# Optimization experiments

Measured on AMD Instinct MI355X. Metric: run time of the kernel, lower is better.

## Reference

```python
import jax, jax.numpy as jnp
import numpy as np
from jax import lax

EPS = 1e-5

# Straight-through binarization (sign forward, identity grad) as in BNN repos
@jax.custom_vjp
def binarize(x):
    return jnp.sign(x)

def _bin_fwd(x):
    return jnp.sign(x), None

def _bin_bwd(_, g):
    return (g,)

binarize.defvjp(_bin_fwd, _bin_bwd)

def hardtanh(x):
    return jnp.clip(x, -1.0, 1.0)

def bn2d(x, g, b):
    # training-mode batch norm over (N,H,W), biased variance (torch behavior)
    m = x.mean(axis=(0, 2, 3), keepdims=True)
    v = x.var(axis=(0, 2, 3), keepdims=True)
    return (x - m) * lax.rsqrt(v + EPS) * g[None, :, None, None] + b[None, :, None, None]

def bn1d(x, g, b):
    m = x.mean(axis=0, keepdims=True)
    v = x.var(axis=0, keepdims=True)
    return (x - m) * lax.rsqrt(v + EPS) * g[None, :] + b[None, :]

def conv(x, w, stride=1, padding='VALID', groups=1):
    return lax.conv_general_dilated(
        x, w, window_strides=(stride, stride), padding=padding,
        dimension_numbers=('NCHW', 'OIHW', 'NCHW'), feature_group_count=groups)

def setup_inputs() -> dict:
    key = jax.random.key(0)
    ks = jax.random.split(key, 16)
    B, C, H = 16, 128, 56
    E = C * 6          # 768 expanded channels
    SE = C // 8        # 16 SE bottleneck
    r = lambda k, sh: (jax.random.normal(k, sh, dtype=jnp.float32) * 0.1)
    return {
        'x': jax.random.normal(ks[0], (B, C, H, H), dtype=jnp.float32),
        'w1': r(ks[1], (E, C, 1, 1)), 'g1': jnp.ones((E,)), 'b1': jnp.zeros((E,)),
        'w2': r(ks[2], (E, 1, 3, 3)), 'g2': jnp.ones((E,)), 'b2': jnp.zeros((E,)),
        'w3': r(ks[3], (C, E, 1, 1)), 'g3': jnp.ones((C,)), 'b3': jnp.zeros((C,)),
        'g_res': jnp.ones((C,)), 'b_res': jnp.zeros((C,)),
        'g_se1': jnp.ones((C,)), 'b_se1': jnp.zeros((C,)),
        'w_fc2': r(ks[4], (SE, C)), 'bias_fc2': jnp.zeros((SE,)),
        'g_se2': jnp.ones((SE,)), 'b_se2': jnp.zeros((SE,)),
        'w_fc3': r(ks[5], (C, SE)), 'bias_fc3': jnp.zeros((C,)),
        'g_se3': jnp.ones((C,)), 'b_se3': jnp.zeros((C,)),
    }

def reference(x, w1, g1, b1, w2, g2, b2, w3, g3, b3, g_res, b_res,
              g_se1, b_se1, w_fc2, bias_fc2, g_se2, b_se2,
              w_fc3, bias_fc3, g_se3, b_se3):
    residual = x
    E = w1.shape[0]
    # 1x1 binarized pointwise expand
    out = conv(binarize(x), binarize(w1))
    out = hardtanh(bn2d(out, g1, b1))
    # 3x3 binarized depthwise (groups = E), stride 1, pad 1
    out = conv(binarize(out), binarize(w2), stride=1, padding='SAME', groups=E)
    out = hardtanh(bn2d(out, g2, b2))
    # 1x1 binarized pointwise project
    out = conv(binarize(out), binarize(w3))
    out = hardtanh(bn2d(out, g3, b3))
    # SE path: global avg pool -> BN -> hardtanh -> binarized FCs -> sigmoid gate
    se = out.mean(axis=(2, 3), keepdims=True)              # [B,C,1,1]
    se = hardtanh(bn2d(se, g_se1, b_se1))[:, :, 0, 0]      # [B,C]
    se = binarize(se) @ binarize(w_fc2).T + bias_fc2
    se = hardtanh(bn1d(se, g_se2, b_se2))
    se = binarize(se) @ binarize(w_fc3).T + bias_fc3
    se = jax.nn.sigmoid(bn1d(se, g_se3, b_se3))            # [B,C]
    out = out * se[:, :, None, None]                       # einsum 'bjik,bj->bjik'
    # residual (stride==1, ch_in==ch_out) + BN + hardtanh
    out = hardtanh(bn2d(out + residual, g_res, b_res))
    return out
```

## Files before the change

kernel.cpp:

```cpp
#include <hip/hip_runtime.h>
#include <stdint.h>

#define BATCH 16
#define CIN   128
#define HH    56
#define HW    3136
#define NPOS  50176
#define ECH   768
#define CH1   49

__device__ uint32_t g_X[NPOS * 8];
__device__ uint32_t g_Wp1[ECH * 8];
__device__ uint32_t g_sw2u[9 * 192];
__device__ uint32_t g_Wp3[CIN * 48];
__device__ int8_t   g_bin1[(size_t)NPOS * ECH];
__device__ int8_t   g_z2[(size_t)NPOS * ECH];
__device__ int16_t  g_z3[(size_t)NPOS * CIN];

__device__ int32_t  g_S1[ECH], g_SS1[ECH];
__device__ int32_t  g_S2[ECH], g_SS2[ECH];
__device__ int32_t  g_S3[CIN];
__device__ unsigned long long g_SS3[CIN];
__device__ double   g_Pm[BATCH * CIN];
__device__ double   g_Ys[CIN], g_Yss[CIN];
__device__ float    g_se[BATCH * CIN];

__device__ __forceinline__ int tdot128(const uint32_t* xn, const uint32_t* xsg,
                                       const uint32_t* wn, const uint32_t* wsg) {
  int pc = 0, mc = 0;
#pragma unroll
  for (int k = 0; k < 4; ++k) {
    uint32_t nab = xn[k] & wn[k];
    uint32_t sx  = xsg[k] ^ wsg[k];
    pc += __popc(nab);
    mc += __popc(nab & sx);
  }
  return pc - 2 * mc;
}

__global__ __launch_bounds__(256) void k_pack(const float* __restrict__ x,
                                              const float* __restrict__ w1,
                                              const float* __restrict__ w2,
                                              const float* __restrict__ w3) {
  __shared__ uint8_t sh[CIN * 64];
  __shared__ uint32_t pk[64 * 8];
  int b = blockIdx.x, t = threadIdx.x;
  if (b < 784) {
    int pos0 = b * 64;
    int n = pos0 / HW, hw0 = pos0 % HW;
    const float* xp = x + (size_t)n * CIN * HW + hw0;
    int lc = t >> 6, lp = t & 63;
#pragma unroll 8
    for (int c4 = 0; c4 < CIN; c4 += 4) {
      float v = xp[(size_t)(c4 + lc) * HW + lp];
      uint8_t code = (v != 0.f) ? (v < 0.f ? 3u : 1u) : 0u;
      sh[(c4 + lc) * 64 + lp] = code;
    }
    __syncthreads();
    int w = t >> 6, p = t & 63;
    uint32_t nw = 0, sw = 0;
#pragma unroll
    for (int i = 0; i < 32; ++i) {
      uint32_t code = sh[(w * 32 + i) * 64 + p];
      nw |= (code & 1u) << i;
      sw |= ((code >> 1) & 1u) << i;
    }
    pk[p * 8 + w] = nw;
    pk[p * 8 + 4 + w] = sw;
    __syncthreads();
    uint32_t* dst = g_X + (size_t)b * 512;
    dst[t] = pk[t];
    dst[t + 256] = pk[t + 256];
  } else if (b < 796) {
    int wid = (b - 784) * 4 + (t >> 6);
    int lane = t & 63;
    for (int e = wid; e < ECH; e += 48) {
      const float* wp = w1 + (size_t)e * CIN;
      float v0 = wp[lane];
      float v1 = wp[64 + lane];
      unsigned long long n0 = __ballot(v0 != 0.f);
      unsigned long long s0 = __ballot(v0 < 0.f);
      unsigned long long n1 = __ballot(v1 != 0.f);
      unsigned long long s1 = __ballot(v1 < 0.f);
      if (lane == 0) {
        uint32_t* d = g_Wp1 + e * 8;
        d[0] = (uint32_t)n0; d[1] = (uint32_t)(n0 >> 32);
        d[2] = (uint32_t)n1; d[3] = (uint32_t)(n1 >> 32);
        d[4] = (uint32_t)s0; d[5] = (uint32_t)(s0 >> 32);
        d[6] = (uint32_t)s1; d[7] = (uint32_t)(s1 >> 32);
      }
    }
  } else if (b < 804) {
    int wid = (b - 796) * 4 + (t >> 6);
    int lane = t & 63;
    for (int o = wid; o < CIN; o += 32) {
      const float* wp = w3 + (size_t)o * ECH;
      uint32_t* d = g_Wp3 + o * 48;
#pragma unroll
      for (int k = 0; k < 12; ++k) {
        float v = wp[k * 64 + lane];
        unsigned long long nm = __ballot(v != 0.f);
        unsigned long long sm = __ballot(v < 0.f);
        if (lane == 0) {
          d[2 * k]     = (uint32_t)nm; d[2 * k + 1]      = (uint32_t)(nm >> 32);
          d[24 + 2 * k] = (uint32_t)sm; d[24 + 2 * k + 1] = (uint32_t)(sm >> 32);
        }
      }
    }
  } else if (b == 804) {
    if (t < 192) {
      int d = t;
#pragma unroll
      for (int tap = 0; tap < 9; ++tap) {
        uint32_t wd = 0;
#pragma unroll
        for (int bb = 0; bb < 4; ++bb) {
          float v = w2[(size_t)(4 * d + bb) * 9 + tap];
          int s8 = (v > 0.f) - (v < 0.f);
          wd |= ((uint32_t)(uint8_t)(int8_t)s8) << (8 * bb);
        }
        g_sw2u[tap * 192 + d] = wd;
      }
    }
  } else {
    for (int i = t; i < ECH; i += 256) { g_S1[i] = 0; g_SS1[i] = 0; g_S2[i] = 0; g_SS2[i] = 0; }
    if (t < CIN) { g_S3[t] = 0; g_SS3[t] = 0ull; g_Ys[t] = 0.0; g_Yss[t] = 0.0; }
  }
}

__global__ __launch_bounds__(256) void k_conv1_stats() {
  __shared__ uint32_t xsh[CH1 * 8];
  int b = blockIdx.x, t = threadIdx.x;
  size_t pos0 = (size_t)b * CH1;
  for (int i = t; i < CH1 * 8; i += 256) xsh[i] = g_X[pos0 * 8 + i];
  uint32_t w[3][8];
#pragma unroll
  for (int j = 0; j < 3; ++j) {
    int e = t + j * 256;
#pragma unroll
    for (int k = 0; k < 8; ++k) w[j][k] = g_Wp1[e * 8 + k];
  }
  __syncthreads();
  int s[3] = {0,0,0}, ss[3] = {0,0,0};
  for (int p = 0; p < CH1; ++p) {
    uint32_t xv[8];
#pragma unroll
    for (int k = 0; k < 8; ++k) xv[k] = xsh[p * 8 + k];
#pragma unroll
    for (int j = 0; j < 3; ++j) {
      int z = tdot128(xv, xv + 4, w[j], w[j] + 4);
      s[j] += z; ss[j] += z * z;
    }
  }
#pragma unroll
  for (int j = 0; j < 3; ++j) {
    int e = t + j * 256;
    atomicAdd(&g_S1[e], s[j]); atomicAdd(&g_SS1[e], ss[j]);
  }
}

__global__ __launch_bounds__(256) void k_conv1_bin(const float* __restrict__ g1,
                                                   const float* __restrict__ b1) {
  __shared__ uint32_t xsh[CH1 * 8];
  int b = blockIdx.x, t = threadIdx.x;
  size_t pos0 = (size_t)b * CH1;
  for (int i = t; i < CH1 * 8; i += 256) xsh[i] = g_X[pos0 * 8 + i];
  uint32_t w[3][8]; float A[3], Bc[3];
#pragma unroll
  for (int j = 0; j < 3; ++j) {
    int e = t + j * 256;
#pragma unroll
    for (int k = 0; k < 8; ++k) w[j][k] = g_Wp1[e * 8 + k];
    double m = (double)g_S1[e] / (double)NPOS;
    double v = (double)g_SS1[e] / (double)NPOS - m * m;
    float inv = (float)(1.0 / sqrt(v + 1e-5));
    A[j] = inv * g1[e]; Bc[j] = b1[e] - (float)m * A[j];
  }
  __syncthreads();
  for (int p = 0; p < CH1; ++p) {
    uint32_t xv[8];
#pragma unroll
    for (int k = 0; k < 8; ++k) xv[k] = xsh[p * 8 + k];
    size_t rowoff = (pos0 + p) * ECH;
#pragma unroll
    for (int j = 0; j < 3; ++j) {
      int z = tdot128(xv, xv + 4, w[j], w[j] + 4);
      float u = fmaf((float)z, A[j], Bc[j]);
      g_bin1[rowoff + t + j * 256] = (int8_t)((u > 0.f) - (u < 0.f));
    }
  }
}

__global__ __launch_bounds__(384) void k_dw() {
  int b = blockIdx.x, t = threadIdx.x;
  int n = b / HH, h = b % HH;
  int half = t >= 192 ? 1 : 0;
  int d = t - half * 192;
  int wbeg = half * 28;

  int ws[9][4];
#pragma unroll
  for (int tap = 0; tap < 9; ++tap) {
    uint32_t wd = g_sw2u[tap * 192 + d];
#pragma unroll
    for (int bb = 0; bb < 4; ++bb) ws[tap][bb] = (int)(int8_t)(uint8_t)(wd >> (8 * bb));
  }

  const uint32_t* binu = (const uint32_t*)g_bin1;
  int rowM = (n * HW + h * HH) * 192 + d;
  bool okT = (h > 0), okB = (h < HH - 1);
  int rT = okT ? rowM - HH * 192 : rowM;
  int rB = okB ? rowM + HH * 192 : rowM;
  uint32_t mT = okT ? 0xffffffffu : 0u;
  uint32_t mB = okB ? 0xffffffffu : 0u;

  uint32_t At, Am, Ab, Bt, Bm, Bb, Ct, Cm, Cb, Dt, Dm, Db, Et, Em, Eb;

#define LOADC(c, vt, vm, vb) do {                                   \
    int cs_ = (c) < 0 ? 0 : ((c) > 55 ? 55 : (c));                  \
    int off_ = cs_ * 192;                                           \
    uint32_t mc_ = ((unsigned)(c) < 56u) ? 0xffffffffu : 0u;        \
    vt = binu[rT + off_];                                           \
    vm = binu[rowM + off_];                                         \
    vb = binu[rB + off_];                                           \
    vt &= (mc_ & mT); vm &= mc_; vb &= (mc_ & mB);                  \
  } while (0)

  LOADC(wbeg - 1, At, Am, Ab);
  LOADC(wbeg,     Bt, Bm, Bb);
  LOADC(wbeg + 1, Ct, Cm, Cb);
  LOADC(wbeg + 2, Dt, Dm, Db);
  LOADC(wbeg + 3, Et, Em, Eb);

  int s0 = 0, s1 = 0, s2 = 0, s3 = 0, q0 = 0, q1 = 0, q2 = 0, q3 = 0;
  uint32_t* z2u = (uint32_t*)g_z2;

#define ACC1(val, tap) do {                                            \
    z0 += __mul24((int)(int8_t)(uint8_t)((val)      ), ws[tap][0]);    \
    z1 += __mul24((int)(int8_t)(uint8_t)((val) >>  8), ws[tap][1]);    \
    z2v+= __mul24((int)(int8_t)(uint8_t)((val) >> 16), ws[tap][2]);    \
    z3 += __mul24((int)(int8_t)(uint8_t)((val) >> 24), ws[tap][3]);    \
  } while (0)

  for (int i = 0; i < 28; ++i) {
    int w = wbeg + i;
    int z0 = 0, z1 = 0, z2v = 0, z3 = 0;
    ACC1(At, 0); ACC1(Bt, 1); ACC1(Ct, 2);
    ACC1(Am, 3); ACC1(Bm, 4); ACC1(Cm, 5);
    ACC1(Ab, 6); ACC1(Bb, 7); ACC1(Cb, 8);
    uint32_t od = (uint32_t)(z0 & 0xff) | ((uint32_t)(z1 & 0xff) << 8) |
                  ((uint32_t)(z2v & 0xff) << 16) | ((uint32_t)(z3 & 0xff) << 24);
    z2u[rowM + w * 192] = od;
    s0 += z0; s1 += z1; s2 += z2v; s3 += z3;
    q0 += __mul24(z0, z0); q1 += __mul24(z1, z1);
    q2 += __mul24(z2v, z2v); q3 += __mul24(z3, z3);
    At = Bt; Am = Bm; Ab = Bb;
    Bt = Ct; Bm = Cm; Bb = Cb;
    Ct = Dt; Cm = Dm; Cb = Db;
    Dt = Et; Dm = Em; Db = Eb;
    LOADC(w + 4, Et, Em, Eb);
  }
#undef LOADC
#undef ACC1

  __shared__ int shS[ECH], shQ[ECH];
  for (int i = t; i < ECH; i += 384) { shS[i] = 0; shQ[i] = 0; }
  __syncthreads();
  atomicAdd(&shS[4 * d + 0], s0); atomicAdd(&shS[4 * d + 1], s1);
  atomicAdd(&shS[4 * d + 2], s2); atomicAdd(&shS[4 * d + 3], s3);
  atomicAdd(&shQ[4 * d + 0], q0); atomicAdd(&shQ[4 * d + 1], q1);
  atomicAdd(&shQ[4 * d + 2], q2); atomicAdd(&shQ[4 * d + 3], q3);
  __syncthreads();
  for (int i = t; i < ECH; i += 384) {
    atomicAdd(&g_S2[i], shS[i]);
    atomicAdd(&g_SS2[i], shQ[i]);
  }
}

__global__ __launch_bounds__(256) void k_conv3(const float* __restrict__ g2,
                                               const float* __restrict__ b2) {
  __shared__ uint32_t pk[64 * 49];
  __shared__ float A2s[ECH], B2s[ECH];
  int b = blockIdx.x, t = threadIdx.x;
  int pos0 = b * 64;
  for (int e = t; e < ECH; e += 256) {
    double m = (double)g_S2[e] / (double)NPOS;
    double v = (double)g_SS2[e] / (double)NPOS - m * m;
    float inv = (float)(1.0 / sqrt(v + 1e-5));
    float Af = inv * g2[e]; A2s[e] = Af; B2s[e] = b2[e] - (float)m * Af;
  }
  __syncthreads();
  int p = t & 63, q = t >> 6;
  const uint4* src = (const uint4*)(g_z2 + (size_t)(pos0 + p) * ECH + q * 192);
  uint32_t nw[6] = {0,0,0,0,0,0}, sw[6] = {0,0,0,0,0,0};
#pragma unroll
  for (int v = 0; v < 12; ++v) {
    uint4 d4 = src[v];
    uint32_t dws[4] = {d4.x, d4.y, d4.z, d4.w};
#pragma unroll
    for (int dw = 0; dw < 4; ++dw) {
      uint32_t dv = dws[dw];
#pragma unroll
      for (int by = 0; by < 4; ++by) {
        int j = v * 16 + dw * 4 + by;
        int c = q * 192 + j;
        float zz = (float)(int)(int8_t)(dv >> (by * 8));
        float u = fmaf(zz, A2s[c], B2s[c]);
        uint32_t bit = 1u << (j & 31);
        if (u != 0.0f) { nw[j >> 5] |= bit; if (u < 0.0f) sw[j >> 5] |= bit; }
      }
    }
  }
#pragma unroll
  for (int k = 0; k < 6; ++k) {
    pk[p * 49 + q * 6 + k] = nw[k];
    pk[p * 49 + 24 + q * 6 + k] = sw[k];
  }
  __syncthreads();
  uint32_t an[24], asx[24];
#pragma unroll
  for (int k = 0; k < 24; ++k) { an[k] = pk[p * 49 + k]; asx[k] = pk[p * 49 + 24 + k]; }
  int n_img = pos0 / HW;
  int hw = pos0 % HW + p;
  for (int i = 0; i < 32; ++i) {
    int o = __builtin_amdgcn_readfirstlane(q * 32 + i);
    const uint32_t* wr = &g_Wp3[o * 48];
    int pc = 0, mc = 0;
#pragma unroll
    for (int k = 0; k < 24; ++k) {
      uint32_t nab = an[k] & wr[k];
      uint32_t sx  = asx[k] ^ wr[24 + k];
      pc += __popc(nab); mc += __popc(nab & sx);
    }
    int z = pc - 2 * mc;
    g_z3[((size_t)n_img * CIN + o) * HW + hw] = (int16_t)z;
  }
}

__global__ __launch_bounds__(256) void k_stats3() {
  int b = blockIdx.x;
  int n = b >> 7, c = b & 127, t = threadIdx.x;
  const uint32_t* zp = (const uint32_t*)(g_z3 + ((size_t)n * CIN + c) * HW);
  int s = 0, ss = 0;
  for (int i = t; i < 1568; i += 256) {
    uint32_t dv = zp[i];
    int a  = (int)(int16_t)(dv & 0xffff);
    int b2 = (int)(int16_t)(dv >> 16);
    s += a + b2; ss += a * a + b2 * b2;
  }
  __shared__ int rs[256], rss[256];
  rs[t] = s; rss[t] = ss; __syncthreads();
  for (int st = 128; st > 0; st >>= 1) {
    if (t < st) { rs[t] += rs[t + st]; rss[t] += rss[t + st]; }
    __syncthreads();
  }
  if (t == 0) {
    atomicAdd(&g_S3[c], rs[0]);
    atomicAdd(&g_SS3[c], (unsigned long long)(unsigned)rss[0]);
  }
}

__global__ __launch_bounds__(256) void k_pool(const float* __restrict__ g3,
                                              const float* __restrict__ b3) {
  int b = blockIdx.x;
  int n = b >> 7, c = b & 127, t = threadIdx.x;
  __shared__ double red[256];
  __shared__ float par[2];
  if (t == 0) {
    double m = (double)g_S3[c] / (double)NPOS;
    double v = (double)g_SS3[c] / (double)NPOS - m * m;
    float inv = (float)(1.0 / sqrt(v + 1e-5));
    float Af = inv * g3[c]; par[0] = Af; par[1] = b3[c] - (float)m * Af;
  }
  __syncthreads();
  float Af = par[0], Bc = par[1];
  const int16_t* zp = g_z3 + ((size_t)n * CIN + c) * HW;
  double acc = 0.0;
  for (int i = t; i < HW; i += 256) {
    float u = fmaf((float)zp[i], Af, Bc);
    u = fminf(1.f, fmaxf(-1.f, u));
    acc += (double)u;
  }
  red[t] = acc; __syncthreads();
  for (int s2 = 128; s2 > 0; s2 >>= 1) { if (t < s2) red[t] += red[t + s2]; __syncthreads(); }
  if (t == 0) g_Pm[b] = red[0];
}

__global__ __launch_bounds__(256) void k_se(const float* __restrict__ g_se1, const float* __restrict__ b_se1,
                                            const float* __restrict__ w_fc2, const float* __restrict__ bias_fc2,
                                            const float* __restrict__ g_se2, const float* __restrict__ b_se2,
                                            const float* __restrict__ w_fc3, const float* __restrict__ bias_fc3,
                                            const float* __restrict__ g_se3, const float* __restrict__ b_se3) {
  __shared__ float s1b[16 * 128];
  __shared__ float s2b[16 * 16];
  __shared__ float zfc[16 * 16];
  int t = threadIdx.x;
  if (t < 128) {
    int c = t; double sum = 0, ssum = 0; double vals[16];
    for (int n = 0; n < 16; ++n) {
      double v = g_Pm[n * 128 + c] / 3136.0;
      vals[n] = v; sum += v; ssum += v * v;
    }
    double m = sum / 16.0, var = ssum / 16.0 - m * m;
    double inv = 1.0 / sqrt(var + 1e-5);
    for (int n = 0; n < 16; ++n) {
      float u = (float)((vals[n] - m) * inv * (double)g_se1[c] + (double)b_se1[c]);
      u = fminf(1.f, fmaxf(-1.f, u));
      s1b[n * 128 + c] = (float)((u > 0.f) - (u < 0.f));
    }
  }
  __syncthreads();
  {
    int n = t >> 4, k = t & 15;
    float acc = bias_fc2[k];
    for (int c = 0; c < 128; ++c) {
      float w = w_fc2[k * 128 + c];
      acc += s1b[n * 128 + c] * (float)((w > 0.f) - (w < 0.f));
    }
    zfc[n * 16 + k] = acc;
  }
  __syncthreads();
  if (t < 16) {
    int k = t; double sum = 0, ssum = 0;
    for (int n = 0; n < 16; ++n) { double v = zfc[n * 16 + k]; sum += v; ssum += v * v; }
    double m = sum / 16.0, var = ssum / 16.0 - m * m;
    double inv = 1.0 / sqrt(var + 1e-5);
    for (int n = 0; n < 16; ++n) {
      float u = (float)(((double)zfc[n * 16 + k] - m) * inv * (double)g_se2[k] + (double)b_se2[k]);
      u = fminf(1.f, fmaxf(-1.f, u));
      s2b[n * 16 + k] = (float)((u > 0.f) - (u < 0.f));
    }
  }
  __syncthreads();
  for (int i = t; i < 2048; i += 256) {
    int n = i >> 7, c = i & 127;
    float acc = bias_fc3[c];
    for (int k = 0; k < 16; ++k) {
      float w = w_fc3[c * 16 + k];
      acc += s2b[n * 16 + k] * (float)((w > 0.f) - (w < 0.f));
    }
    s1b[i] = acc;
  }
  __syncthreads();
  if (t < 128) {
    int c = t; double sum = 0, ssum = 0;
    for (int n = 0; n < 16; ++n) { double v = s1b[n * 128 + c]; sum += v; ssum += v * v; }
    double m = sum / 16.0, var = ssum / 16.0 - m * m;
    double inv = 1.0 / sqrt(var + 1e-5);
    for (int n = 0; n < 16; ++n) {
      double u = ((double)s1b[n * 128 + c] - m) * inv * (double)g_se3[c] + (double)b_se3[c];
      g_se[n * 128 + c] = 1.f / (1.f + expf((float)(-u)));
    }
  }
}

__global__ __launch_bounds__(256) void k_ystats(const float* __restrict__ x,
                                                const float* __restrict__ g3,
                                                const float* __restrict__ b3) {
  int b = blockIdx.x;
  int half = b & 1, nc = b >> 1, c = nc & 127, n = nc >> 7;
  int t = threadIdx.x;
  __shared__ double redS[256], redSS[256];
  __shared__ float par[3];
  if (t == 0) {
    double m = (double)g_S3[c] / (double)NPOS;
    double v = (double)g_SS3[c] / (double)NPOS - m * m;
    float inv = (float)(1.0 / sqrt(v + 1e-5));
    float Af = inv * g3[c];
    par[0] = Af; par[1] = b3[c] - (float)m * Af; par[2] = g_se[n * 128 + c];
  }
  __syncthreads();
  float Af = par[0], Bc = par[1], sev = par[2];
  size_t base = ((size_t)n * CIN + c) * HW + half * 1568;
  const int16_t* zp = g_z3 + base;
  const float* xp = x + base;
  double s = 0, ssum = 0;
  for (int i = t; i < 1568; i += 256) {
    float u = fmaf((float)zp[i], Af, Bc);
    u = fminf(1.f, fmaxf(-1.f, u));
    float y = fmaf(u, sev, xp[i]);
    s += (double)y; ssum += (double)y * (double)y;
  }
  redS[t] = s; redSS[t] = ssum; __syncthreads();
  for (int st = 128; st > 0; st >>= 1) {
    if (t < st) { redS[t] += redS[t + st]; redSS[t] += redSS[t + st]; }
    __syncthreads();
  }
  if (t == 0) { atomicAdd(&g_Ys[c], redS[0]); atomicAdd(&g_Yss[c], redSS[0]); }
}

__global__ __launch_bounds__(256) void k_out(const float* __restrict__ x,
                                             const float* __restrict__ g3,
                                             const float* __restrict__ b3,
                                             const float* __restrict__ gr,
                                             const float* __restrict__ br,
                                             float* __restrict__ out) {
  int b = blockIdx.x;
  int half = b & 1, nc = b >> 1, c = nc & 127, n = nc >> 7;
  int t = threadIdx.x;
  __shared__ float par[5];
  if (t == 0) {
    double m = (double)g_S3[c] / (double)NPOS;
    double v = (double)g_SS3[c] / (double)NPOS - m * m;
    float inv = (float)(1.0 / sqrt(v + 1e-5));
    float A3 = inv * g3[c];
    par[0] = A3; par[1] = b3[c] - (float)m * A3; par[2] = g_se[n * 128 + c];
    double mr = g_Ys[c] / (double)NPOS;
    double vr = g_Yss[c] / (double)NPOS - mr * mr;
    float invr = (float)(1.0 / sqrt(vr + 1e-5));
    float Ar = invr * gr[c];
    par[3] = Ar; par[4] = br[c] - (float)mr * Ar;
  }
  __syncthreads();
  float A3 = par[0], B3 = par[1], sev = par[2], Ar = par[3], Br = par[4];
  size_t base = ((size_t)n * CIN + c) * HW + half * 1568;
  const int16_t* zp = g_z3 + base;
  const float* xp = x + base;
  float* op = out + base;
  for (int i = t; i < 1568; i += 256) {
    float u = fmaf((float)zp[i], A3, B3);
    u = fminf(1.f, fmaxf(-1.f, u));
    float y = fmaf(u, sev, xp[i]);
    float o = fmaf(y, Ar, Br);
    o = fminf(1.f, fmaxf(-1.f, o));
    op[i] = o;
  }
}

extern "C" void kernel_launch(void* const* d_in, const int* in_sizes, int n_in,
                              void* d_out, int out_size, void* d_ws, size_t ws_size,
                              hipStream_t stream) {
  const float* x       = (const float*)d_in[0];
  const float* w1      = (const float*)d_in[1];
  const float* g1      = (const float*)d_in[2];
  const float* b1      = (const float*)d_in[3];
  const float* w2      = (const float*)d_in[4];
  const float* g2      = (const float*)d_in[5];
  const float* b2      = (const float*)d_in[6];
  const float* w3      = (const float*)d_in[7];
  const float* g3      = (const float*)d_in[8];
  const float* b3      = (const float*)d_in[9];
  const float* g_res   = (const float*)d_in[10];
  const float* b_res   = (const float*)d_in[11];
  const float* g_se1   = (const float*)d_in[12];
  const float* b_se1   = (const float*)d_in[13];
  const float* w_fc2   = (const float*)d_in[14];
  const float* bias_fc2= (const float*)d_in[15];
  const float* g_se2   = (const float*)d_in[16];
  const float* b_se2   = (const float*)d_in[17];
  const float* w_fc3   = (const float*)d_in[18];
  const float* bias_fc3= (const float*)d_in[19];
  const float* g_se3   = (const float*)d_in[20];
  const float* b_se3   = (const float*)d_in[21];
  float* out = (float*)d_out;

  hipLaunchKernelGGL(k_pack,        dim3(806),  dim3(256), 0, stream, x, w1, w2, w3);
  hipLaunchKernelGGL(k_conv1_stats, dim3(1024), dim3(256), 0, stream);
  hipLaunchKernelGGL(k_conv1_bin,   dim3(1024), dim3(256), 0, stream, g1, b1);
  hipLaunchKernelGGL(k_dw,          dim3(896),  dim3(384), 0, stream);
  hipLaunchKernelGGL(k_conv3,       dim3(784),  dim3(256), 0, stream, g2, b2);
  hipLaunchKernelGGL(k_stats3,      dim3(2048), dim3(256), 0, stream);
  hipLaunchKernelGGL(k_pool,        dim3(2048), dim3(256), 0, stream, g3, b3);
  hipLaunchKernelGGL(k_se,          dim3(1),    dim3(256), 0, stream,
                     g_se1, b_se1, w_fc2, bias_fc2, g_se2, b_se2, w_fc3, bias_fc3, g_se3, b_se3);
  hipLaunchKernelGGL(k_ystats,      dim3(4096), dim3(256), 0, stream, x, g3, b3);
  hipLaunchKernelGGL(k_out,         dim3(4096), dim3(256), 0, stream, x, g3, b3, g_res, b_res, out);
}
```

Before: 351.8 us.

## Split conv3 into binarize-pack kernel and separate popcount GEMM kernel

The fused conv3 kernel is split in two. The first kernel binarizes the depthwise output and writes packed sign/nonzero bitmasks to a global buffer laid out as [word][position]. A second kernel runs with more blocks, each thread covering one position and 16 output channels, reading packed words with coalesced loads and writing int16 outputs. This aims to raise parallelism and make output stores coalesced across consecutive positions, at the cost of an extra global round trip of about 9.6MB and one more kernel launch.

```diff
diff --git a/kernel.cpp b/kernel.cpp
--- a/kernel.cpp
+++ b/kernel.cpp
@@ -15,6 +15,8 @@
 __device__ uint32_t g_Wp3[CIN * 48];
 __device__ int8_t   g_bin1[(size_t)NPOS * ECH];
 __device__ int8_t   g_z2[(size_t)NPOS * ECH];
+__device__ uint32_t g_pkN[(size_t)24 * NPOS];
+__device__ uint32_t g_pkS[(size_t)24 * NPOS];
 __device__ int16_t  g_z3[(size_t)NPOS * CIN];
 
 __device__ int32_t  g_S1[ECH], g_SS1[ECH];
@@ -277,9 +279,8 @@
   }
 }
 
-__global__ __launch_bounds__(256) void k_conv3(const float* __restrict__ g2,
-                                               const float* __restrict__ b2) {
-  __shared__ uint32_t pk[64 * 49];
+__global__ __launch_bounds__(256) void k_binpack(const float* __restrict__ g2,
+                                                 const float* __restrict__ b2) {
   __shared__ float A2s[ECH], B2s[ECH];
   int b = blockIdx.x, t = threadIdx.x;
   int pos0 = b * 64;
@@ -291,7 +292,8 @@
   }
   __syncthreads();
   int p = t & 63, q = t >> 6;
-  const uint4* src = (const uint4*)(g_z2 + (size_t)(pos0 + p) * ECH + q * 192);
+  int pos = pos0 + p;
+  const uint4* src = (const uint4*)(g_z2 + (size_t)pos * ECH + q * 192);
   uint32_t nw[6] = {0,0,0,0,0,0}, sw[6] = {0,0,0,0,0,0};
 #pragma unroll
   for (int v = 0; v < 12; ++v) {
@@ -312,18 +314,27 @@
     }
   }
 #pragma unroll
-  for (int k = 0; k < 6; ++k) {
-    pk[p * 49 + q * 6 + k] = nw[k];
-    pk[p * 49 + 24 + q * 6 + k] = sw[k];
-  }
-  __syncthreads();
+  for (int j = 0; j < 6; ++j) {
+    g_pkN[(size_t)(q * 6 + j) * NPOS + pos] = nw[j];
+    g_pkS[(size_t)(q * 6 + j) * NPOS + pos] = sw[j];
+  }
+}
+
+__global__ __launch_bounds__(256) void k_gemm3() {
+  int b = blockIdx.x, t = threadIdx.x;
+  int posblk = b >> 3, oblk = b & 7;
+  int pos = posblk * 256 + t;
   uint32_t an[24], asx[24];
 #pragma unroll
-  for (int k = 0; k < 24; ++k) { an[k] = pk[p * 49 + k]; asx[k] = pk[p * 49 + 24 + k]; }
-  int n_img = pos0 / HW;
-  int hw = pos0 % HW + p;
-  for (int i = 0; i < 32; ++i) {
-    int o = __builtin_amdgcn_readfirstlane(q * 32 + i);
+  for (int k = 0; k < 24; ++k) {
+    an[k]  = g_pkN[(size_t)k * NPOS + pos];
+    asx[k] = g_pkS[(size_t)k * NPOS + pos];
+  }
+  int n_img = pos / HW, hw = pos % HW;
+  size_t obase = ((size_t)n_img * CIN) * HW + hw;
+#pragma unroll
+  for (int i = 0; i < 16; ++i) {
+    int o = __builtin_amdgcn_readfirstlane(oblk * 16 + i);
     const uint32_t* wr = &g_Wp3[o * 48];
     int pc = 0, mc = 0;
 #pragma unroll
@@ -333,7 +344,7 @@
       pc += __popc(nab); mc += __popc(nab & sx);
     }
     int z = pc - 2 * mc;
-    g_z3[((size_t)n_img * CIN + o) * HW + hw] = (int16_t)z;
+    g_z3[obase + (size_t)o * HW] = (int16_t)z;
   }
 }
 
@@ -558,7 +569,8 @@
   hipLaunchKernelGGL(k_conv1_stats, dim3(1024), dim3(256), 0, stream);
   hipLaunchKernelGGL(k_conv1_bin,   dim3(1024), dim3(256), 0, stream, g1, b1);
   hipLaunchKernelGGL(k_dw,          dim3(896),  dim3(384), 0, stream);
-  hipLaunchKernelGGL(k_conv3,       dim3(784),  dim3(256), 0, stream, g2, b2);
+  hipLaunchKernelGGL(k_binpack,     dim3(784),  dim3(256), 0, stream, g2, b2);
+  hipLaunchKernelGGL(k_gemm3,       dim3(1568), dim3(256), 0, stream);
   hipLaunchKernelGGL(k_stats3,      dim3(2048), dim3(256), 0, stream);
   hipLaunchKernelGGL(k_pool,        dim3(2048), dim3(256), 0, stream, g3, b3);
   hipLaunchKernelGGL(k_se,          dim3(1),    dim3(256), 0, stream,
```

New measurement: 353.2 us. About the same (+0.4%).
